# Optimization experiments

Measured on AMD Instinct MI355X. Metric: run time of the kernel, lower is better.

Reference implementation:

```python
import jax, jax.numpy as jnp
import numpy as np
import math

TOTAL_RANK = 16
ACTIVE_RANK = 8
HADAMARD_DIM = 16
ADAPT_DIM = 32
HIDDEN = 2048
LN_EPS = 1e-5


def _hadamard(n: int) -> np.ndarray:
    # Replicates the module's recursive construction (normalizes by sqrt(n) at EVERY level).
    if n == 1:
        return np.array([[1.0]], dtype=np.float32)
    h = _hadamard(n // 2)
    return (np.block([[h, h], [h, -h]]) / math.sqrt(n)).astype(np.float32)


def setup_inputs() -> dict:
    key = jax.random.key(0)
    ks = jax.random.split(key, 8)
    B, S = 8, 4096
    hidden_states = jax.random.normal(ks[0], (B, S, HIDDEN), dtype=jnp.float32)
    rank_activations = jax.random.normal(ks[1], (B, S, TOTAL_RANK), dtype=jnp.float32)
    W1 = jax.random.normal(ks[2], (HIDDEN, ADAPT_DIM), dtype=jnp.float32) / math.sqrt(HIDDEN)
    b1 = jnp.zeros((ADAPT_DIM,), dtype=jnp.float32)
    ln_gamma = jnp.ones((ADAPT_DIM,), dtype=jnp.float32)
    ln_beta = jnp.zeros((ADAPT_DIM,), dtype=jnp.float32)
    W2 = jax.random.normal(ks[3], (ADAPT_DIM, TOTAL_RANK), dtype=jnp.float32) / math.sqrt(ADAPT_DIM)
    b2 = jnp.zeros((TOTAL_RANK,), dtype=jnp.float32)
    mask_logits = jax.random.normal(ks[4], (TOTAL_RANK,), dtype=jnp.float32) * 0.1
    rank_scales = jnp.ones((TOTAL_RANK,), dtype=jnp.float32)
    return {
        "hidden_states": hidden_states,
        "rank_activations": rank_activations,
        "W1": W1, "b1": b1, "ln_gamma": ln_gamma, "ln_beta": ln_beta,
        "W2": W2, "b2": b2, "mask_logits": mask_logits, "rank_scales": rank_scales,
    }


def reference(hidden_states, rank_activations, W1, b1, ln_gamma, ln_beta, W2, b2,
              mask_logits, rank_scales):
    B = hidden_states.shape[0]
    # Instance-adaptive logits: adaptation_net(hidden.mean(dim=1)) — eval mode (dropout off).
    pooled = jnp.mean(hidden_states, axis=1)                      # [B, H]
    x = pooled @ W1 + b1                                          # [B, A]
    mu = jnp.mean(x, axis=-1, keepdims=True)
    var = jnp.var(x, axis=-1, keepdims=True)
    x = (x - mu) * jax.lax.rsqrt(var + LN_EPS) * ln_gamma + ln_beta
    x = jax.nn.gelu(x, approximate=False)
    instance_logits = x @ W2 + b2                                 # [B, R]
    combined = instance_logits + mask_logits[None, :]
    # k-hot mask via top-k + scatter (eval path)
    _, idx = jax.lax.top_k(combined, ACTIVE_RANK)                 # [B, k]
    mask = jnp.zeros_like(combined).at[jnp.arange(B)[:, None], idx].set(1.0)
    # mask + scale
    scaled = rank_activations * mask[:, None, :] * rank_scales[None, None, :]  # [B,S,R]
    # Hadamard path: total_rank == hadamard_dim == 16 -> no padding, slice is no-op.
    H = jnp.asarray(_hadamard(HADAMARD_DIM))
    transformed = jnp.einsum('bsr,dr->bsd', scaled, H)            # x @ H.T
    final = transformed[:, :, :TOTAL_RANK]
    return final
```

## Files before the change

kernel.cpp:

```cpp
#include <hip/hip_runtime.h>
#include <hip/hip_bf16.h>
#include <math.h>

#define S_LEN   4096
#define HID     2048
#define NB      8
#define SC      64
#define S_PER   (S_LEN / SC)
#define R       16
#define AD      32

__global__ void pool_proj(const float* __restrict__ hs,
                          const float* __restrict__ W1,
                          float* __restrict__ xpart) {
    __shared__ float hsum[HID];
    __shared__ float cpart[8][AD];
    int t  = threadIdx.x;
    int sc = blockIdx.x;
    int b  = blockIdx.y;

    const float* base = hs + ((size_t)b * S_LEN + (size_t)sc * S_PER) * HID;
    const float* p0 = base + t * 4;
    const float* p1 = base + 1024 + t * 4;
    float4 a0 = make_float4(0.f, 0.f, 0.f, 0.f);
    float4 a1 = make_float4(0.f, 0.f, 0.f, 0.f);
#pragma unroll 8
    for (int s = 0; s < S_PER; ++s) {
        float4 v0 = *(const float4*)(p0 + (size_t)s * HID);
        float4 v1 = *(const float4*)(p1 + (size_t)s * HID);
        a0.x += v0.x; a0.y += v0.y; a0.z += v0.z; a0.w += v0.w;
        a1.x += v1.x; a1.y += v1.y; a1.z += v1.z; a1.w += v1.w;
    }
    *(float4*)&hsum[t * 4]        = a0;
    *(float4*)&hsum[1024 + t * 4] = a1;
    __syncthreads();

    int j = t & 31, g = t >> 5;
    const float* w = W1 + (size_t)(g * 256) * AD + j;
    float c = 0.f;
#pragma unroll 4
    for (int k = 0; k < 256; ++k)
        c += hsum[g * 256 + k] * w[(size_t)k * AD];
    cpart[g][j] = c;
    __syncthreads();

    if (t < AD) {
        float s = 0.f;
#pragma unroll
        for (int gg = 0; gg < 8; ++gg) s += cpart[gg][t];
        xpart[((size_t)(b * SC + sc)) * AD + t] = s;
    }
}

__global__ void controller2(const float* __restrict__ xpart,
                            const float* __restrict__ b1,
                            const float* __restrict__ gamma,
                            const float* __restrict__ beta,
                            const float* __restrict__ W2,
                            const float* __restrict__ b2v,
                            const float* __restrict__ mlog,
                            const float* __restrict__ rsc,
                            float* __restrict__ maskscale) {
    __shared__ float xp[8][AD];
    __shared__ float xv[AD];
    __shared__ float xg[AD];
    __shared__ float comb[R];
    int b = blockIdx.x, t = threadIdx.x;
    int j = t & 31, g = t >> 5;

    const float* xb = xpart + (size_t)b * SC * AD;
    float s = 0.f;
#pragma unroll
    for (int r = 0; r < 8; ++r) s += xb[(size_t)(g * 8 + r) * AD + j];
    xp[g][j] = s;
    __syncthreads();

    if (t < AD) {
        float x = 0.f;
#pragma unroll
        for (int gg = 0; gg < 8; ++gg) x += xp[gg][t];
        xv[t] = x * (1.0f / (float)S_LEN) + b1[t];
    }
    __syncthreads();

    if (t < AD) {
        float mu = 0.f;
#pragma unroll
        for (int k = 0; k < AD; ++k) mu += xv[k];
        mu *= (1.0f / AD);
        float var = 0.f;
#pragma unroll
        for (int k = 0; k < AD; ++k) { float d = xv[k] - mu; var += d * d; }
        var *= (1.0f / AD);
        float x = (xv[t] - mu) * rsqrtf(var + 1e-5f) * gamma[t] + beta[t];
        xg[t] = 0.5f * x * (1.0f + erff(x * 0.70710678118654752f));
    }
    __syncthreads();

    if (t < R) {
        float lg = b2v[t];
#pragma unroll
        for (int k = 0; k < AD; ++k) lg += xg[k] * W2[(size_t)k * R + t];
        comb[t] = lg + mlog[t];
    }
    __syncthreads();

    if (t < R) {
        float v = comb[t];
        int cnt = 0;
#pragma unroll
        for (int k = 0; k < R; ++k)
            cnt += (comb[k] > v) || (comb[k] == v && k < t);
        maskscale[b * R + t] = (cnt < 8) ? rsc[t] : 0.f;
    }
}

__global__ void apply_hadamard(const float* __restrict__ ra,
                               const float* __restrict__ maskscale,
                               float* __restrict__ out) {
    __shared__ float ms[R];
    int t = threadIdx.x;
    int blk = blockIdx.x;
    int b = blk >> 4;
    if (t < R) ms[t] = maskscale[b * R + t];
    __syncthreads();

    size_t row = (size_t)blk * 256 + t;
    const float* src = ra + row * R;
    float a[R];
#pragma unroll
    for (int i = 0; i < 4; ++i) {
        float4 v = ((const float4*)src)[i];
        a[4 * i + 0] = v.x; a[4 * i + 1] = v.y;
        a[4 * i + 2] = v.z; a[4 * i + 3] = v.w;
    }
#pragma unroll
    for (int r = 0; r < R; ++r) a[r] *= ms[r];

#pragma unroll
    for (int hstep = 1; hstep < R; hstep <<= 1) {
#pragma unroll
        for (int i = 0; i < R; ++i) {
            if ((i & hstep) == 0) {
                float u = a[i], v = a[i | hstep];
                a[i] = u + v; a[i | hstep] = u - v;
            }
        }
    }

    float* dst = out + row * R;
#pragma unroll
    for (int i = 0; i < 4; ++i) {
        float4 v;
        v.x = a[4 * i + 0] * 0.03125f; v.y = a[4 * i + 1] * 0.03125f;
        v.z = a[4 * i + 2] * 0.03125f; v.w = a[4 * i + 3] * 0.03125f;
        ((float4*)dst)[i] = v;
    }
}

extern "C" void kernel_launch(void* const* d_in, const int* in_sizes, int n_in,
                              void* d_out, int out_size, void* d_ws, size_t ws_size,
                              hipStream_t stream) {
    const float* hs    = (const float*)d_in[0];
    const float* ra    = (const float*)d_in[1];
    const float* W1    = (const float*)d_in[2];
    const float* b1    = (const float*)d_in[3];
    const float* gamma = (const float*)d_in[4];
    const float* beta  = (const float*)d_in[5];
    const float* W2    = (const float*)d_in[6];
    const float* b2v   = (const float*)d_in[7];
    const float* mlog  = (const float*)d_in[8];
    const float* rsc   = (const float*)d_in[9];
    float* out = (float*)d_out;

    float* xpart     = (float*)d_ws;
    float* maskscale = xpart + (size_t)NB * SC * AD;

    pool_proj     <<<dim3(SC, NB), 256, 0, stream>>>(hs, W1, xpart);
    controller2   <<<NB, 256, 0, stream>>>(xpart, b1, gamma, beta,
                                           W2, b2v, mlog, rsc, maskscale);
    apply_hadamard<<<128, 256, 0, stream>>>(ra, maskscale, out);
}
```

Baseline: 65.30 us.

## Fuse controller into Hadamard kernel, double pooling split, use nontemporal accesses

Merges the controller and Hadamard apply kernels into one launch in which each of 256 blocks of 128 threads recomputes its batch's mask from the pooled partials. This removes one kernel launch and the maskscale round trip through memory. The pooling grid doubles to 128 sequence chunks per batch to raise parallelism on the 256 MB streaming read, and the large streams now use nontemporal loads and stores. In exchange, the small controller math is done redundantly in every block, and the partial buffer the controller reads is twice as large.

After: 56.85 us. 12.9% less time.

```diff
diff --git a/kernel.cpp b/kernel.cpp
--- a/kernel.cpp
+++ b/kernel.cpp
@@ -5,10 +5,12 @@
 #define S_LEN   4096
 #define HID     2048
 #define NB      8
-#define SC      64
+#define SC      128
 #define S_PER   (S_LEN / SC)
 #define R       16
 #define AD      32
+
+typedef float f4 __attribute__((ext_vector_type(4)));
 
 __global__ void pool_proj(const float* __restrict__ hs,
                           const float* __restrict__ W1,
@@ -20,19 +22,19 @@
     int b  = blockIdx.y;
 
     const float* base = hs + ((size_t)b * S_LEN + (size_t)sc * S_PER) * HID;
-    const float* p0 = base + t * 4;
-    const float* p1 = base + 1024 + t * 4;
-    float4 a0 = make_float4(0.f, 0.f, 0.f, 0.f);
-    float4 a1 = make_float4(0.f, 0.f, 0.f, 0.f);
+    const f4* p0 = (const f4*)(base + t * 4);
+    const f4* p1 = (const f4*)(base + 1024 + t * 4);
+    f4 a0 = (f4)(0.f);
+    f4 a1 = (f4)(0.f);
 #pragma unroll 8
     for (int s = 0; s < S_PER; ++s) {
-        float4 v0 = *(const float4*)(p0 + (size_t)s * HID);
-        float4 v1 = *(const float4*)(p1 + (size_t)s * HID);
-        a0.x += v0.x; a0.y += v0.y; a0.z += v0.z; a0.w += v0.w;
-        a1.x += v1.x; a1.y += v1.y; a1.z += v1.z; a1.w += v1.w;
+        f4 v0 = __builtin_nontemporal_load(p0 + (size_t)s * (HID / 4));
+        f4 v1 = __builtin_nontemporal_load(p1 + (size_t)s * (HID / 4));
+        a0 += v0;
+        a1 += v1;
     }
-    *(float4*)&hsum[t * 4]        = a0;
-    *(float4*)&hsum[1024 + t * 4] = a1;
+    *(f4*)&hsum[t * 4]        = a0;
+    *(f4*)&hsum[1024 + t * 4] = a1;
     __syncthreads();
 
     int j = t & 31, g = t >> 5;
@@ -52,33 +54,37 @@
     }
 }
 
-__global__ void controller2(const float* __restrict__ xpart,
-                            const float* __restrict__ b1,
-                            const float* __restrict__ gamma,
-                            const float* __restrict__ beta,
-                            const float* __restrict__ W2,
-                            const float* __restrict__ b2v,
-                            const float* __restrict__ mlog,
-                            const float* __restrict__ rsc,
-                            float* __restrict__ maskscale) {
-    __shared__ float xp[8][AD];
+__global__ void ctrl_hadamard(const float* __restrict__ xpart,
+                              const float* __restrict__ b1,
+                              const float* __restrict__ gamma,
+                              const float* __restrict__ beta,
+                              const float* __restrict__ W2,
+                              const float* __restrict__ b2v,
+                              const float* __restrict__ mlog,
+                              const float* __restrict__ rsc,
+                              const float* __restrict__ ra,
+                              float* __restrict__ out) {
+    __shared__ float xp[4][AD];
     __shared__ float xv[AD];
     __shared__ float xg[AD];
     __shared__ float comb[R];
-    int b = blockIdx.x, t = threadIdx.x;
+    __shared__ float ms[R];
+    int t   = threadIdx.x;
+    int blk = blockIdx.x;
+    int b   = blk >> 5;
+
     int j = t & 31, g = t >> 5;
-
     const float* xb = xpart + (size_t)b * SC * AD;
     float s = 0.f;
-#pragma unroll
-    for (int r = 0; r < 8; ++r) s += xb[(size_t)(g * 8 + r) * AD + j];
+#pragma unroll 8
+    for (int r = 0; r < 32; ++r) s += xb[(size_t)(g * 32 + r) * AD + j];
     xp[g][j] = s;
     __syncthreads();
 
     if (t < AD) {
         float x = 0.f;
 #pragma unroll
-        for (int gg = 0; gg < 8; ++gg) x += xp[gg][t];
+        for (int gg = 0; gg < 4; ++gg) x += xp[gg][t];
         xv[t] = x * (1.0f / (float)S_LEN) + b1[t];
     }
     __syncthreads();
@@ -111,26 +117,16 @@
 #pragma unroll
         for (int k = 0; k < R; ++k)
             cnt += (comb[k] > v) || (comb[k] == v && k < t);
-        maskscale[b * R + t] = (cnt < 8) ? rsc[t] : 0.f;
+        ms[t] = (cnt < 8) ? rsc[t] : 0.f;
     }
-}
-
-__global__ void apply_hadamard(const float* __restrict__ ra,
-                               const float* __restrict__ maskscale,
-                               float* __restrict__ out) {
-    __shared__ float ms[R];
-    int t = threadIdx.x;
-    int blk = blockIdx.x;
-    int b = blk >> 4;
-    if (t < R) ms[t] = maskscale[b * R + t];
     __syncthreads();
 
-    size_t row = (size_t)blk * 256 + t;
-    const float* src = ra + row * R;
+    size_t row = (size_t)blk * 128 + t;
+    const f4* src = (const f4*)(ra + row * R);
     float a[R];
 #pragma unroll
     for (int i = 0; i < 4; ++i) {
-        float4 v = ((const float4*)src)[i];
+        f4 v = __builtin_nontemporal_load(src + i);
         a[4 * i + 0] = v.x; a[4 * i + 1] = v.y;
         a[4 * i + 2] = v.z; a[4 * i + 3] = v.w;
     }
@@ -148,13 +144,13 @@
         }
     }
 
-    float* dst = out + row * R;
+    f4* dst = (f4*)(out + row * R);
 #pragma unroll
     for (int i = 0; i < 4; ++i) {
-        float4 v;
+        f4 v;
         v.x = a[4 * i + 0] * 0.03125f; v.y = a[4 * i + 1] * 0.03125f;
         v.z = a[4 * i + 2] * 0.03125f; v.w = a[4 * i + 3] * 0.03125f;
-        ((float4*)dst)[i] = v;
+        __builtin_nontemporal_store(v, dst + i);
     }
 }
 
@@ -173,11 +169,9 @@
     const float* rsc   = (const float*)d_in[9];
     float* out = (float*)d_out;
 
-    float* xpart     = (float*)d_ws;
-    float* maskscale = xpart + (size_t)NB * SC * AD;
+    float* xpart = (float*)d_ws;
 
-    pool_proj     <<<dim3(SC, NB), 256, 0, stream>>>(hs, W1, xpart);
-    controller2   <<<NB, 256, 0, stream>>>(xpart, b1, gamma, beta,
-                                           W2, b2v, mlog, rsc, maskscale);
-    apply_hadamard<<<128, 256, 0, stream>>>(ra, maskscale, out);
+    pool_proj    <<<dim3(SC, NB), 256, 0, stream>>>(hs, W1, xpart);
+    ctrl_hadamard<<<256, 128, 0, stream>>>(xpart, b1, gamma, beta,
+                                           W2, b2v, mlog, rsc, ra, out);
 }
```
